# Kernel tuning notes

Measured on AMD Instinct MI355X. Metric: run time of the kernel, lower is better.

Reference implementation:

```python
import jax, jax.numpy as jnp
import numpy as np

N, E = 100000, 1600000
D_IN, D_HID, D_OUT = 128, 128, 64


def setup_inputs() -> dict:
    key = jax.random.key(0)
    ks = jax.random.split(key, 12)
    x = jax.random.normal(ks[0], (N, D_IN), dtype=jnp.float32)
    edge_index = jax.random.randint(ks[1], (2, E), 0, N, dtype=jnp.int32)

    def glorot(k, fan_in, fan_out):
        lim = np.sqrt(6.0 / (fan_in + fan_out)).astype(np.float32)
        return jax.random.uniform(k, (fan_in, fan_out), jnp.float32, -lim, lim)

    return {
        "x": x,
        "edge_index": edge_index,
        "W_l0": glorot(ks[2], D_IN, D_HID), "W_r0": glorot(ks[3], D_IN, D_HID), "b0": jnp.zeros((D_HID,), jnp.float32),
        "W_l1": glorot(ks[4], D_HID, D_HID), "W_r1": glorot(ks[5], D_HID, D_HID), "b1": jnp.zeros((D_HID,), jnp.float32),
        "W_l2": glorot(ks[6], D_HID, D_OUT), "W_r2": glorot(ks[7], D_HID, D_OUT), "b2": jnp.zeros((D_OUT,), jnp.float32),
    }


def _sage_conv(x, src, dst, W_l, W_r, b):
    # mean aggregation of source features onto destination nodes
    msg = jnp.take(x, src, axis=0)                               # [E, d]
    agg = jax.ops.segment_sum(msg, dst, num_segments=N)          # [N, d]
    deg = jax.ops.segment_sum(jnp.ones_like(dst, x.dtype), dst, num_segments=N)
    agg = agg / jnp.maximum(deg, 1.0)[:, None]
    # out = lin_l(aggr) + lin_r(x); lin_l has bias (PyG SAGEConv convention)
    return agg @ W_l + x @ W_r + b


def reference(x, edge_index, W_l0, W_r0, b0, W_l1, W_r1, b1, W_l2, W_r2, b2):
    src, dst = edge_index[0], edge_index[1]
    h = jax.nn.relu(_sage_conv(x, src, dst, W_l0, W_r0, b0))
    h = jax.nn.relu(_sage_conv(h, src, dst, W_l1, W_r1, b1))
    # dropout is identity in eval mode
    return _sage_conv(h, src, dst, W_l2, W_r2, b2)
```

## Files before the change

kernel.cpp:

```cpp
#include <hip/hip_runtime.h>
#include <hip/hip_bf16.h>
#include <stdint.h>

#define D 128
#define BSH 8
#define BKN 256
#define TILE 4096
#define CAPB 5376

typedef __attribute__((ext_vector_type(8))) short short8;
typedef __attribute__((ext_vector_type(4))) float f32x4;

typedef __attribute__((address_space(1))) const void gvoid;
typedef __attribute__((address_space(3))) void lvoid;

__device__ inline float bf16lo(uint32_t u){ return __uint_as_float(u << 16); }
__device__ inline float bf16hi(uint32_t u){ return __uint_as_float(u & 0xffff0000u); }
__device__ inline unsigned short f2bf(float f){
    union { __hip_bfloat16 h; unsigned short u; } cvt;
    cvt.h = __float2bfloat16(f);
    return cvt.u;
}

#define ACC8(q) \
    acc[0] += bf16lo(q.x); acc[1] += bf16hi(q.x); \
    acc[2] += bf16lo(q.y); acc[3] += bf16hi(q.y); \
    acc[4] += bf16lo(q.z); acc[5] += bf16hi(q.z); \
    acc[6] += bf16lo(q.w); acc[7] += bf16hi(q.w);

#define ACC4(q) \
    acc[0] += bf16lo(q.x); acc[1] += bf16hi(q.x); \
    acc[2] += bf16lo(q.y); acc[3] += bf16hi(q.y);

__global__ __launch_bounds__(256) void bin_edges(
    const int* __restrict__ src, const int* __restrict__ dst,
    int* __restrict__ bfill, uint32_t* __restrict__ binbuf, int E, int nbk)
{
    __shared__ int hist[400];
    __shared__ int cur[400];
    int t = threadIdx.x;
    int tile0 = blockIdx.x * TILE;
    int cnt = min(TILE, E - tile0);

    for (int i = t; i < nbk; i += 256) hist[i] = 0;
    __syncthreads();
    for (int i = t; i < cnt; i += 256)
        atomicAdd(&hist[dst[tile0 + i] >> BSH], 1);
    __syncthreads();
    for (int i = t; i < nbk; i += 256){
        int h = hist[i];
        int base = h ? atomicAdd(&bfill[i], h) : 0;
        cur[i] = i * CAPB + base;
    }
    __syncthreads();
    for (int i = t; i < cnt; i += 256){
        int d = dst[tile0 + i];
        int b = d >> BSH;
        int p = atomicAdd(&cur[b], 1);
        binbuf[p] = (uint32_t)src[tile0 + i] | ((uint32_t)(d & (BKN - 1)) << 17);
    }
}

__global__ __launch_bounds__(256) void fill_bucket(
    const uint32_t* __restrict__ binbuf, const int* __restrict__ bcnt,
    int* __restrict__ roff, int* __restrict__ rend, int* __restrict__ csr, int n, int nbk)
{
    __shared__ int hist[BKN];
    __shared__ int hist2[BKN];
    __shared__ int hb[BKN];
    __shared__ int sc[256];
    int b = blockIdx.x, t = threadIdx.x;
    int e0 = b * CAPB;
    int e1 = e0 + bcnt[b];
    int v0 = b << BSH;
    int nv = min(BKN, n - v0);

    hist[t] = 0; hist2[t] = 0;
    __syncthreads();
    for (int e = e0 + t; e < e1; e += 256)
        atomicAdd(&hist[binbuf[e] >> 17], 1);
    __syncthreads();
    int own = hist[t];
    sc[t] = own;
    __syncthreads();
    for (int o = 1; o < 256; o <<= 1){
        int x = (t >= o) ? sc[t - o] : 0;
        __syncthreads();
        sc[t] += x;
        __syncthreads();
    }
    int ex = sc[t] - own;
    hb[t] = ex;
    if (t < nv){
        roff[v0 + t] = e0 + ex;
        rend[v0 + t] = e0 + ex + own;
    }
    __syncthreads();
    for (int e = e0 + t; e < e1; e += 256){
        uint32_t p = binbuf[e];
        int local = p >> 17;
        int pos = e0 + hb[local] + atomicAdd(&hist2[local], 1);
        csr[pos] = (int)(p & 0x1FFFFu);
    }
}

__global__ void wt_prep(const float* __restrict__ Wl, const float* __restrict__ Wr,
                        unsigned short* __restrict__ WT, int dout){
    int nc = dout * 2;
    int idx = blockIdx.x * 256 + threadIdx.x;
    if (idx >= nc * 128) return;
    int k = idx & 127, j = idx >> 7;
    float w = (j < dout) ? Wl[k * dout + j] : Wr[k * dout + (j - dout)];
    WT[j * 128 + k] = f2bf(w);
}

template<int NC, bool AF32>
__global__ __launch_bounds__(256, 3) void dense_gemm(
    const unsigned short* __restrict__ xb, const float* __restrict__ xf,
    const unsigned short* __restrict__ WT, const float* __restrict__ bias,
    unsigned short* __restrict__ ylz, int n)
{
    constexpr int DOUT = NC / 2;
    __shared__ __align__(16) char As[128 * 256];
    int tid = threadIdx.x, lane = tid & 63, wave = tid >> 6;
    int rbase = blockIdx.x * 128;
    int lrow = lane & 15, lk = (lane >> 4) * 8;
    int colbase = blockIdx.y * 128 + wave * 32;

    short8 bfr[4][2];
    #pragma unroll
    for (int kk = 0; kk < 4; kk++)
        #pragma unroll
        for (int cf = 0; cf < 2; cf++)
            bfr[kk][cf] = *reinterpret_cast<const short8*>(
                WT + (size_t)(colbase + cf * 16 + lrow) * 128 + kk * 32 + lk);

    if constexpr (AF32){
        int cb = (tid & 15) * 16;
        #pragma unroll
        for (int i = 0; i < 8; i++){
            int row = i * 16 + (tid >> 4);
            int grow = min(rbase + row, n - 1);
            const float* p = xf + (size_t)grow * 128 + (cb >> 1);
            float4 f0 = *reinterpret_cast<const float4*>(p);
            float4 f1 = *reinterpret_cast<const float4*>(p + 4);
            uint4 q;
            q.x = (uint32_t)f2bf(f0.x) | ((uint32_t)f2bf(f0.y) << 16);
            q.y = (uint32_t)f2bf(f0.z) | ((uint32_t)f2bf(f0.w) << 16);
            q.z = (uint32_t)f2bf(f1.x) | ((uint32_t)f2bf(f1.y) << 16);
            q.w = (uint32_t)f2bf(f1.z) | ((uint32_t)f2bf(f1.w) << 16);
            *reinterpret_cast<uint4*>(As + row * 256 + (cb ^ ((row & 7) << 4))) = q;
        }
    } else {
        int cb = (lane & 15) * 16;
        #pragma unroll
        for (int i = 0; i < 8; i++){
            int row = i * 16 + (tid >> 4);
            int grow = min(rbase + row, n - 1);
            const unsigned short* gsrc = xb + (size_t)grow * 128 + ((cb ^ ((row & 7) << 4)) >> 1);
            __builtin_amdgcn_global_load_lds(
                (gvoid*)gsrc,
                (lvoid*)(As + (i * 16 + wave * 4) * 256),
                16, 0, 0);
        }
    }
    __syncthreads();

    f32x4 acc[8][2];
    #pragma unroll
    for (int fr = 0; fr < 8; fr++)
        #pragma unroll
        for (int cf = 0; cf < 2; cf++)
            acc[fr][cf] = (f32x4){0.f, 0.f, 0.f, 0.f};

    #pragma unroll
    for (int kk = 0; kk < 4; kk++){
        int cb = kk * 64 + (lane >> 4) * 16;
        #pragma unroll
        for (int fr = 0; fr < 8; fr++){
            int row = fr * 16 + lrow;
            short8 a = *reinterpret_cast<const short8*>(As + row * 256 + (cb ^ ((row & 7) << 4)));
            #pragma unroll
            for (int cf = 0; cf < 2; cf++)
                acc[fr][cf] = __builtin_amdgcn_mfma_f32_16x16x32_bf16(bfr[kk][cf], a, acc[fr][cf], 0, 0, 0);
        }
    }

    float4 bv[2];
    #pragma unroll
    for (int cf = 0; cf < 2; cf++){
        int cg = colbase + cf * 16 + (lane >> 4) * 4;
        bv[cf] = (cg >= DOUT) ? *reinterpret_cast<const float4*>(bias + (cg - DOUT))
                              : (float4){0.f, 0.f, 0.f, 0.f};
    }

    #pragma unroll
    for (int fr = 0; fr < 8; fr++){
        int row = rbase + fr * 16 + lrow;
        if (row < n){
            #pragma unroll
            for (int cf = 0; cf < 2; cf++){
                int cg = colbase + cf * 16 + (lane >> 4) * 4;
                uint2 o;
                o.x = (uint32_t)f2bf(acc[fr][cf][0] + bv[cf].x) |
                      ((uint32_t)f2bf(acc[fr][cf][1] + bv[cf].y) << 16);
                o.y = (uint32_t)f2bf(acc[fr][cf][2] + bv[cf].z) |
                      ((uint32_t)f2bf(acc[fr][cf][3] + bv[cf].w) << 16);
                *reinterpret_cast<uint2*>(ylz + (size_t)row * NC + cg) = o;
            }
        }
    }
}

__global__ __launch_bounds__(256, 6) void agg_relu(
    const unsigned short* __restrict__ ylz, const int* __restrict__ roff,
    const int* __restrict__ rend,
    const int* __restrict__ csr, unsigned short* __restrict__ hout, int n)
{
    int grp = threadIdx.x >> 4, li = threadIdx.x & 15;
    int v = blockIdx.x * 16 + grp;
    if (v >= n) return;
    int s0 = roff[v], s1 = rend[v];
    const unsigned short* base = ylz + li * 8;
    float acc[8] = {0.f,0.f,0.f,0.f,0.f,0.f,0.f,0.f};
    int e = s0;
    for (; e + 8 <= s1; e += 8){
        int i0=csr[e],i1=csr[e+1],i2=csr[e+2],i3=csr[e+3];
        int i4=csr[e+4],i5=csr[e+5],i6=csr[e+6],i7=csr[e+7];
        uint4 q0 = *reinterpret_cast<const uint4*>(base + (size_t)i0 * 256);
        uint4 q1 = *reinterpret_cast<const uint4*>(base + (size_t)i1 * 256);
        uint4 q2 = *reinterpret_cast<const uint4*>(base + (size_t)i2 * 256);
        uint4 q3 = *reinterpret_cast<const uint4*>(base + (size_t)i3 * 256);
        uint4 q4 = *reinterpret_cast<const uint4*>(base + (size_t)i4 * 256);
        uint4 q5 = *reinterpret_cast<const uint4*>(base + (size_t)i5 * 256);
        uint4 q6 = *reinterpret_cast<const uint4*>(base + (size_t)i6 * 256);
        uint4 q7 = *reinterpret_cast<const uint4*>(base + (size_t)i7 * 256);
        ACC8(q0) ACC8(q1) ACC8(q2) ACC8(q3) ACC8(q4) ACC8(q5) ACC8(q6) ACC8(q7)
    }
    if (e < s1){
        int last = s1 - 1;
        int i0=csr[e];
        int i1=csr[min(e+1,last)],i2=csr[min(e+2,last)],i3=csr[min(e+3,last)];
        int i4=csr[min(e+4,last)],i5=csr[min(e+5,last)],i6=csr[min(e+6,last)],i7=csr[min(e+7,last)];
        uint4 z4 = make_uint4(0,0,0,0);
        uint4 q0 = *reinterpret_cast<const uint4*>(base + (size_t)i0 * 256);
        uint4 q1 = *reinterpret_cast<const uint4*>(base + (size_t)i1 * 256);
        uint4 q2 = *reinterpret_cast<const uint4*>(base + (size_t)i2 * 256);
        uint4 q3 = *reinterpret_cast<const uint4*>(base + (size_t)i3 * 256);
        uint4 q4 = *reinterpret_cast<const uint4*>(base + (size_t)i4 * 256);
        uint4 q5 = *reinterpret_cast<const uint4*>(base + (size_t)i5 * 256);
        uint4 q6 = *reinterpret_cast<const uint4*>(base + (size_t)i6 * 256);
        uint4 q7 = *reinterpret_cast<const uint4*>(base + (size_t)i7 * 256);
        if (e+1 > last) q1 = z4;
        if (e+2 > last) q2 = z4;
        if (e+3 > last) q3 = z4;
        if (e+4 > last) q4 = z4;
        if (e+5 > last) q5 = z4;
        if (e+6 > last) q6 = z4;
        if (e+7 > last) q7 = z4;
        ACC8(q0) ACC8(q1) ACC8(q2) ACC8(q3) ACC8(q4) ACC8(q5) ACC8(q6) ACC8(q7)
    }
    int d = s1 - s0;
    float inv = (d > 0) ? 1.0f / (float)d : 0.0f;
    uint4 zq = *reinterpret_cast<const uint4*>(ylz + (size_t)v * 256 + 128 + li * 8);
    float z0=bf16lo(zq.x), z1=bf16hi(zq.x), z2=bf16lo(zq.y), z3=bf16hi(zq.y);
    float z4_=bf16lo(zq.z), z5=bf16hi(zq.z), z6=bf16lo(zq.w), z7=bf16hi(zq.w);
    uint4 o;
    o.x = (uint32_t)f2bf(fmaxf(acc[0]*inv+z0,0.f)) | ((uint32_t)f2bf(fmaxf(acc[1]*inv+z1,0.f)) << 16);
    o.y = (uint32_t)f2bf(fmaxf(acc[2]*inv+z2,0.f)) | ((uint32_t)f2bf(fmaxf(acc[3]*inv+z3,0.f)) << 16);
    o.z = (uint32_t)f2bf(fmaxf(acc[4]*inv+z4_,0.f)) | ((uint32_t)f2bf(fmaxf(acc[5]*inv+z5,0.f)) << 16);
    o.w = (uint32_t)f2bf(fmaxf(acc[6]*inv+z6,0.f)) | ((uint32_t)f2bf(fmaxf(acc[7]*inv+z7,0.f)) << 16);
    *reinterpret_cast<uint4*>(hout + (size_t)v * 128 + li * 8) = o;
}

__global__ __launch_bounds__(256, 6) void agg_out64(
    const unsigned short* __restrict__ ylz, const int* __restrict__ roff,
    const int* __restrict__ rend,
    const int* __restrict__ csr, float* __restrict__ out, int n)
{
    int grp = threadIdx.x >> 4, li = threadIdx.x & 15;
    int v = blockIdx.x * 16 + grp;
    if (v >= n) return;
    int s0 = roff[v], s1 = rend[v];
    const unsigned short* base = ylz + li * 4;
    float acc[4] = {0.f,0.f,0.f,0.f};
    int e = s0;
    for (; e + 8 <= s1; e += 8){
        int i0=csr[e],i1=csr[e+1],i2=csr[e+2],i3=csr[e+3];
        int i4=csr[e+4],i5=csr[e+5],i6=csr[e+6],i7=csr[e+7];
        uint2 q0 = *reinterpret_cast<const uint2*>(base + (size_t)i0 * 128);
        uint2 q1 = *reinterpret_cast<const uint2*>(base + (size_t)i1 * 128);
        uint2 q2 = *reinterpret_cast<const uint2*>(base + (size_t)i2 * 128);
        uint2 q3 = *reinterpret_cast<const uint2*>(base + (size_t)i3 * 128);
        uint2 q4 = *reinterpret_cast<const uint2*>(base + (size_t)i4 * 128);
        uint2 q5 = *reinterpret_cast<const uint2*>(base + (size_t)i5 * 128);
        uint2 q6 = *reinterpret_cast<const uint2*>(base + (size_t)i6 * 128);
        uint2 q7 = *reinterpret_cast<const uint2*>(base + (size_t)i7 * 128);
        ACC4(q0) ACC4(q1) ACC4(q2) ACC4(q3) ACC4(q4) ACC4(q5) ACC4(q6) ACC4(q7)
    }
    if (e < s1){
        int last = s1 - 1;
        int i0=csr[e];
        int i1=csr[min(e+1,last)],i2=csr[min(e+2,last)],i3=csr[min(e+3,last)];
        int i4=csr[min(e+4,last)],i5=csr[min(e+5,last)],i6=csr[min(e+6,last)],i7=csr[min(e+7,last)];
        uint2 z2_ = make_uint2(0,0);
        uint2 q0 = *reinterpret_cast<const uint2*>(base + (size_t)i0 * 128);
        uint2 q1 = *reinterpret_cast<const uint2*>(base + (size_t)i1 * 128);
        uint2 q2 = *reinterpret_cast<const uint2*>(base + (size_t)i2 * 128);
        uint2 q3 = *reinterpret_cast<const uint2*>(base + (size_t)i3 * 128);
        uint2 q4 = *reinterpret_cast<const uint2*>(base + (size_t)i4 * 128);
        uint2 q5 = *reinterpret_cast<const uint2*>(base + (size_t)i5 * 128);
        uint2 q6 = *reinterpret_cast<const uint2*>(base + (size_t)i6 * 128);
        uint2 q7 = *reinterpret_cast<const uint2*>(base + (size_t)i7 * 128);
        if (e+1 > last) q1 = z2_;
        if (e+2 > last) q2 = z2_;
        if (e+3 > last) q3 = z2_;
        if (e+4 > last) q4 = z2_;
        if (e+5 > last) q5 = z2_;
        if (e+6 > last) q6 = z2_;
        if (e+7 > last) q7 = z2_;
        ACC4(q0) ACC4(q1) ACC4(q2) ACC4(q3) ACC4(q4) ACC4(q5) ACC4(q6) ACC4(q7)
    }
    int d = s1 - s0;
    float inv = (d > 0) ? 1.0f / (float)d : 0.0f;
    uint2 zq = *reinterpret_cast<const uint2*>(ylz + (size_t)v * 128 + 64 + li * 4);
    float4 o;
    o.x = acc[0]*inv + bf16lo(zq.x);
    o.y = acc[1]*inv + bf16hi(zq.x);
    o.z = acc[2]*inv + bf16lo(zq.y);
    o.w = acc[3]*inv + bf16hi(zq.y);
    *reinterpret_cast<float4*>(out + (size_t)v * 64 + li * 4) = o;
}

extern "C" void kernel_launch(void* const* d_in, const int* in_sizes, int n_in,
                              void* d_out, int out_size, void* d_ws, size_t ws_size,
                              hipStream_t stream)
{
    const float* x   = (const float*)d_in[0];
    const int*   ei  = (const int*)d_in[1];
    const float* Wl0 = (const float*)d_in[2];
    const float* Wr0 = (const float*)d_in[3];
    const float* b0  = (const float*)d_in[4];
    const float* Wl1 = (const float*)d_in[5];
    const float* Wr1 = (const float*)d_in[6];
    const float* b1  = (const float*)d_in[7];
    const float* Wl2 = (const float*)d_in[8];
    const float* Wr2 = (const float*)d_in[9];
    const float* b2  = (const float*)d_in[10];

    int N = in_sizes[0] / D;
    int E = in_sizes[1] / 2;
    const int* src = ei;
    const int* dst = ei + E;
    int NBK = (N + BKN - 1) >> BSH;

    char* ws = (char*)d_ws;
    size_t off = 0;
    auto alloc = [&](size_t bytes) -> void* {
        void* p = ws + off;
        off = (off + bytes + 255) & ~(size_t)255;
        return p;
    };
    int*      bfill  = (int*)alloc((size_t)NBK * 4);
    int*      roff   = (int*)alloc((size_t)N * 4);
    int*      rend   = (int*)alloc((size_t)N * 4);
    int*      csr    = (int*)alloc((size_t)NBK * CAPB * 4);
    unsigned short* ylz = (unsigned short*)alloc((size_t)N * 256 * 2);
    unsigned short* h0  = (unsigned short*)alloc((size_t)N * D * 2);
    unsigned short* h1  = (unsigned short*)alloc((size_t)N * D * 2);
    unsigned short* WT0 = (unsigned short*)alloc((size_t)256 * 128 * 2);
    unsigned short* WT1 = (unsigned short*)alloc((size_t)256 * 128 * 2);
    unsigned short* WT2 = (unsigned short*)alloc((size_t)128 * 128 * 2);
    uint32_t* binbuf = (uint32_t*)ylz;

    hipMemsetAsync(bfill, 0, (size_t)NBK * 4, stream);

    bin_edges<<<(E + TILE - 1) / TILE, 256, 0, stream>>>(src, dst, bfill, binbuf, E, NBK);
    fill_bucket<<<NBK, 256, 0, stream>>>(binbuf, bfill, roff, rend, csr, N, NBK);

    wt_prep<<<(256 * 128 + 255) / 256, 256, 0, stream>>>(Wl0, Wr0, WT0, 128);
    wt_prep<<<(256 * 128 + 255) / 256, 256, 0, stream>>>(Wl1, Wr1, WT1, 128);
    wt_prep<<<(128 * 128 + 255) / 256, 256, 0, stream>>>(Wl2, Wr2, WT2, 64);

    int gG = (N + 127) / 128;
    int gA = (N + 15) / 16;

    dense_gemm<256, true ><<<dim3(gG, 2), 256, 0, stream>>>(nullptr, x, WT0, b0, ylz, N);
    agg_relu<<<gA, 256, 0, stream>>>(ylz, roff, rend, csr, h0, N);
    dense_gemm<256, false><<<dim3(gG, 2), 256, 0, stream>>>(h0, nullptr, WT1, b1, ylz, N);
    agg_relu<<<gA, 256, 0, stream>>>(ylz, roff, rend, csr, h1, N);
    dense_gemm<128, false><<<dim3(gG, 1), 256, 0, stream>>>(h1, nullptr, WT2, b2, ylz, N);
    agg_out64<<<gA, 256, 0, stream>>>(ylz, roff, rend, csr, (float*)d_out, N);
}
```

Before: 281.6 us.

## Merge weight prep launches, widen final aggregation loads, lower agg occupancy hint

```diff
diff --git a/kernel.cpp b/kernel.cpp
--- a/kernel.cpp
+++ b/kernel.cpp
@@ -27,10 +27,6 @@
     acc[2] += bf16lo(q.y); acc[3] += bf16hi(q.y); \
     acc[4] += bf16lo(q.z); acc[5] += bf16hi(q.z); \
     acc[6] += bf16lo(q.w); acc[7] += bf16hi(q.w);
-
-#define ACC4(q) \
-    acc[0] += bf16lo(q.x); acc[1] += bf16hi(q.x); \
-    acc[2] += bf16lo(q.y); acc[3] += bf16hi(q.y);
 
 __global__ __launch_bounds__(256) void bin_edges(
     const int* __restrict__ src, const int* __restrict__ dst,
@@ -104,14 +100,24 @@
     }
 }
 
-__global__ void wt_prep(const float* __restrict__ Wl, const float* __restrict__ Wr,
-                        unsigned short* __restrict__ WT, int dout){
-    int nc = dout * 2;
+__global__ void wt_prep_all(
+    const float* __restrict__ Wl0, const float* __restrict__ Wr0,
+    const float* __restrict__ Wl1, const float* __restrict__ Wr1,
+    const float* __restrict__ Wl2, const float* __restrict__ Wr2,
+    unsigned short* __restrict__ WT0, unsigned short* __restrict__ WT1,
+    unsigned short* __restrict__ WT2)
+{
     int idx = blockIdx.x * 256 + threadIdx.x;
-    if (idx >= nc * 128) return;
-    int k = idx & 127, j = idx >> 7;
-    float w = (j < dout) ? Wl[k * dout + j] : Wr[k * dout + (j - dout)];
-    WT[j * 128 + k] = f2bf(w);
+    if (idx < 32768){
+        int k = idx & 127, j = idx >> 7;
+        WT0[j * 128 + k] = f2bf(j < 128 ? Wl0[k * 128 + j] : Wr0[k * 128 + (j - 128)]);
+    } else if (idx < 65536){
+        int i = idx - 32768; int k = i & 127, j = i >> 7;
+        WT1[j * 128 + k] = f2bf(j < 128 ? Wl1[k * 128 + j] : Wr1[k * 128 + (j - 128)]);
+    } else if (idx < 81920){
+        int i = idx - 65536; int k = i & 127, j = i >> 7;
+        WT2[j * 128 + k] = f2bf(j < 64 ? Wl2[k * 64 + j] : Wr2[k * 64 + (j - 64)]);
+    }
 }
 
 template<int NC, bool AF32>
@@ -212,7 +218,7 @@
     }
 }
 
-__global__ __launch_bounds__(256, 6) void agg_relu(
+__global__ __launch_bounds__(256, 4) void agg_relu(
     const unsigned short* __restrict__ ylz, const int* __restrict__ roff,
     const int* __restrict__ rend,
     const int* __restrict__ csr, unsigned short* __restrict__ hout, int n)
@@ -273,63 +279,68 @@
     *reinterpret_cast<uint4*>(hout + (size_t)v * 128 + li * 8) = o;
 }
 
-__global__ __launch_bounds__(256, 6) void agg_out64(
+__global__ __launch_bounds__(256, 4) void agg_out64(
     const unsigned short* __restrict__ ylz, const int* __restrict__ roff,
     const int* __restrict__ rend,
     const int* __restrict__ csr, float* __restrict__ out, int n)
 {
-    int grp = threadIdx.x >> 4, li = threadIdx.x & 15;
-    int v = blockIdx.x * 16 + grp;
+    int grp = threadIdx.x >> 3, li = threadIdx.x & 7;
+    int v = blockIdx.x * 32 + grp;
     if (v >= n) return;
     int s0 = roff[v], s1 = rend[v];
-    const unsigned short* base = ylz + li * 4;
-    float acc[4] = {0.f,0.f,0.f,0.f};
+    const unsigned short* base = ylz + li * 8;
+    float acc[8] = {0.f,0.f,0.f,0.f,0.f,0.f,0.f,0.f};
     int e = s0;
     for (; e + 8 <= s1; e += 8){
         int i0=csr[e],i1=csr[e+1],i2=csr[e+2],i3=csr[e+3];
         int i4=csr[e+4],i5=csr[e+5],i6=csr[e+6],i7=csr[e+7];
-        uint2 q0 = *reinterpret_cast<const uint2*>(base + (size_t)i0 * 128);
-        uint2 q1 = *reinterpret_cast<const uint2*>(base + (size_t)i1 * 128);
-        uint2 q2 = *reinterpret_cast<const uint2*>(base + (size_t)i2 * 128);
-        uint2 q3 = *reinterpret_cast<const uint2*>(base + (size_t)i3 * 128);
-        uint2 q4 = *reinterpret_cast<const uint2*>(base + (size_t)i4 * 128);
-        uint2 q5 = *reinterpret_cast<const uint2*>(base + (size_t)i5 * 128);
-        uint2 q6 = *reinterpret_cast<const uint2*>(base + (size_t)i6 * 128);
-        uint2 q7 = *reinterpret_cast<const uint2*>(base + (size_t)i7 * 128);
-        ACC4(q0) ACC4(q1) ACC4(q2) ACC4(q3) ACC4(q4) ACC4(q5) ACC4(q6) ACC4(q7)
+        uint4 q0 = *reinterpret_cast<const uint4*>(base + (size_t)i0 * 128);
+        uint4 q1 = *reinterpret_cast<const uint4*>(base + (size_t)i1 * 128);
+        uint4 q2 = *reinterpret_cast<const uint4*>(base + (size_t)i2 * 128);
+        uint4 q3 = *reinterpret_cast<const uint4*>(base + (size_t)i3 * 128);
+        uint4 q4 = *reinterpret_cast<const uint4*>(base + (size_t)i4 * 128);
+        uint4 q5 = *reinterpret_cast<const uint4*>(base + (size_t)i5 * 128);
+        uint4 q6 = *reinterpret_cast<const uint4*>(base + (size_t)i6 * 128);
+        uint4 q7 = *reinterpret_cast<const uint4*>(base + (size_t)i7 * 128);
+        ACC8(q0) ACC8(q1) ACC8(q2) ACC8(q3) ACC8(q4) ACC8(q5) ACC8(q6) ACC8(q7)
     }
     if (e < s1){
         int last = s1 - 1;
         int i0=csr[e];
         int i1=csr[min(e+1,last)],i2=csr[min(e+2,last)],i3=csr[min(e+3,last)];
         int i4=csr[min(e+4,last)],i5=csr[min(e+5,last)],i6=csr[min(e+6,last)],i7=csr[min(e+7,last)];
-        uint2 z2_ = make_uint2(0,0);
-        uint2 q0 = *reinterpret_cast<const uint2*>(base + (size_t)i0 * 128);
-        uint2 q1 = *reinterpret_cast<const uint2*>(base + (size_t)i1 * 128);
-        uint2 q2 = *reinterpret_cast<const uint2*>(base + (size_t)i2 * 128);
-        uint2 q3 = *reinterpret_cast<const uint2*>(base + (size_t)i3 * 128);
-        uint2 q4 = *reinterpret_cast<const uint2*>(base + (size_t)i4 * 128);
-        uint2 q5 = *reinterpret_cast<const uint2*>(base + (size_t)i5 * 128);
-        uint2 q6 = *reinterpret_cast<const uint2*>(base + (size_t)i6 * 128);
-        uint2 q7 = *reinterpret_cast<const uint2*>(base + (size_t)i7 * 128);
-        if (e+1 > last) q1 = z2_;
-        if (e+2 > last) q2 = z2_;
-        if (e+3 > last) q3 = z2_;
-        if (e+4 > last) q4 = z2_;
-        if (e+5 > last) q5 = z2_;
-        if (e+6 > last) q6 = z2_;
-        if (e+7 > last) q7 = z2_;
-        ACC4(q0) ACC4(q1) ACC4(q2) ACC4(q3) ACC4(q4) ACC4(q5) ACC4(q6) ACC4(q7)
+        uint4 z4 = make_uint4(0,0,0,0);
+        uint4 q0 = *reinterpret_cast<const uint4*>(base + (size_t)i0 * 128);
+        uint4 q1 = *reinterpret_cast<const uint4*>(base + (size_t)i1 * 128);
+        uint4 q2 = *reinterpret_cast<const uint4*>(base + (size_t)i2 * 128);
+        uint4 q3 = *reinterpret_cast<const uint4*>(base + (size_t)i3 * 128);
+        uint4 q4 = *reinterpret_cast<const uint4*>(base + (size_t)i4 * 128);
+        uint4 q5 = *reinterpret_cast<const uint4*>(base + (size_t)i5 * 128);
+        uint4 q6 = *reinterpret_cast<const uint4*>(base + (size_t)i6 * 128);
+        uint4 q7 = *reinterpret_cast<const uint4*>(base + (size_t)i7 * 128);
+        if (e+1 > last) q1 = z4;
+        if (e+2 > last) q2 = z4;
+        if (e+3 > last) q3 = z4;
+        if (e+4 > last) q4 = z4;
+        if (e+5 > last) q5 = z4;
+        if (e+6 > last) q6 = z4;
+        if (e+7 > last) q7 = z4;
+        ACC8(q0) ACC8(q1) ACC8(q2) ACC8(q3) ACC8(q4) ACC8(q5) ACC8(q6) ACC8(q7)
     }
     int d = s1 - s0;
     float inv = (d > 0) ? 1.0f / (float)d : 0.0f;
-    uint2 zq = *reinterpret_cast<const uint2*>(ylz + (size_t)v * 128 + 64 + li * 4);
-    float4 o;
-    o.x = acc[0]*inv + bf16lo(zq.x);
-    o.y = acc[1]*inv + bf16hi(zq.x);
-    o.z = acc[2]*inv + bf16lo(zq.y);
-    o.w = acc[3]*inv + bf16hi(zq.y);
-    *reinterpret_cast<float4*>(out + (size_t)v * 64 + li * 4) = o;
+    uint4 zq = *reinterpret_cast<const uint4*>(ylz + (size_t)v * 128 + 64 + li * 8);
+    float4 o0, o1;
+    o0.x = acc[0]*inv + bf16lo(zq.x);
+    o0.y = acc[1]*inv + bf16hi(zq.x);
+    o0.z = acc[2]*inv + bf16lo(zq.y);
+    o0.w = acc[3]*inv + bf16hi(zq.y);
+    o1.x = acc[4]*inv + bf16lo(zq.z);
+    o1.y = acc[5]*inv + bf16hi(zq.z);
+    o1.z = acc[6]*inv + bf16lo(zq.w);
+    o1.w = acc[7]*inv + bf16hi(zq.w);
+    *reinterpret_cast<float4*>(out + (size_t)v * 64 + li * 8) = o0;
+    *reinterpret_cast<float4*>(out + (size_t)v * 64 + li * 8 + 4) = o1;
 }
 
 extern "C" void kernel_launch(void* const* d_in, const int* in_sizes, int n_in,
@@ -378,17 +389,16 @@
     bin_edges<<<(E + TILE - 1) / TILE, 256, 0, stream>>>(src, dst, bfill, binbuf, E, NBK);
     fill_bucket<<<NBK, 256, 0, stream>>>(binbuf, bfill, roff, rend, csr, N, NBK);
 
-    wt_prep<<<(256 * 128 + 255) / 256, 256, 0, stream>>>(Wl0, Wr0, WT0, 128);
-    wt_prep<<<(256 * 128 + 255) / 256, 256, 0, stream>>>(Wl1, Wr1, WT1, 128);
-    wt_prep<<<(128 * 128 + 255) / 256, 256, 0, stream>>>(Wl2, Wr2, WT2, 64);
+    wt_prep_all<<<320, 256, 0, stream>>>(Wl0, Wr0, Wl1, Wr1, Wl2, Wr2, WT0, WT1, WT2);
 
     int gG = (N + 127) / 128;
     int gA = (N + 15) / 16;
+    int gA2 = (N + 31) / 32;
 
     dense_gemm<256, true ><<<dim3(gG, 2), 256, 0, stream>>>(nullptr, x, WT0, b0, ylz, N);
     agg_relu<<<gA, 256, 0, stream>>>(ylz, roff, rend, csr, h0, N);
     dense_gemm<256, false><<<dim3(gG, 2), 256, 0, stream>>>(h0, nullptr, WT1, b1, ylz, N);
     agg_relu<<<gA, 256, 0, stream>>>(ylz, roff, rend, csr, h1, N);
     dense_gemm<128, false><<<dim3(gG, 1), 256, 0, stream>>>(h1, nullptr, WT2, b2, ylz, N);
-    agg_out64<<<gA, 256, 0, stream>>>(ylz, roff, rend, csr, (float*)d_out, N);
-}
+    agg_out64<<<gA2, 256, 0, stream>>>(ylz, roff, rend, csr, (float*)d_out, N);
+}
```

Measured after the change: 275.9 us. 1.02x faster.
